# Optimization experiments

Measured on AMD Instinct MI355X. Metric: run time of the kernel, lower is better.

Reference implementation:

```python
import jax, jax.numpy as jnp
import numpy as np

B, N, D, H, E = 32, 512, 512, 8, 4
HD = D // H
EPS = 1e-3  # keras LayerNormalization default epsilon
NEG = -1e9  # keras Softmax masking additive constant


def _ln(x, g, b):
    m = jnp.mean(x, axis=-1, keepdims=True)
    v = jnp.mean(jnp.square(x - m), axis=-1, keepdims=True)
    return (x - m) * jax.lax.rsqrt(v + EPS) * g + b


def setup_inputs() -> dict:
    key = jax.random.key(0)
    ks = jax.random.split(key, 16)
    s = 0.02
    return {
        "x": jax.random.normal(ks[0], (B, N, D), jnp.float32),
        "mask": jax.random.randint(ks[1], (B, 1, N, N), 0, 2) > 0,
        "interaction": jax.random.normal(ks[2], (B, N, N, H), jnp.float32),
        "w_qkv": jax.random.normal(ks[3], (D, 3 * D), jnp.float32) * s,
        "b_qkv": jnp.zeros((3 * D,), jnp.float32),
        "w_out": jax.random.normal(ks[4], (D, D), jnp.float32) * s,
        "b_out": jnp.zeros((D,), jnp.float32),
        "w1": jax.random.normal(ks[5], (D, E * D), jnp.float32) * s,
        "b1": jnp.zeros((E * D,), jnp.float32),
        "w2": jax.random.normal(ks[6], (E * D, D), jnp.float32) * s,
        "b2": jnp.zeros((D,), jnp.float32),
        "g_pre": jnp.ones((D,), jnp.float32), "be_pre": jnp.zeros((D,), jnp.float32),
        "g_post": jnp.ones((D,), jnp.float32), "be_post": jnp.zeros((D,), jnp.float32),
        "g_ffn": jnp.ones((D,), jnp.float32), "be_ffn": jnp.zeros((D,), jnp.float32),
        "g_mid": jnp.ones((E * D,), jnp.float32), "be_mid": jnp.zeros((E * D,), jnp.float32),
    }


def reference(x, mask, interaction, w_qkv, b_qkv, w_out, b_out, w1, b1, w2, b2,
              g_pre, be_pre, g_post, be_post, g_ffn, be_ffn, g_mid, be_mid):
    # pre-LN MHSA
    h = _ln(x, g_pre, be_pre)
    qkv = h @ w_qkv + b_qkv                           # [B,N,3D]
    qkv = qkv.reshape(B, N, 3, H, HD)
    q, k, v = (jnp.transpose(qkv[:, :, i], (0, 2, 1, 3)) for i in range(3))  # [B,H,N,HD]
    scores = jnp.einsum('bhnd,bhmd->bhnm', q, k) / np.sqrt(HD).astype(np.float32)
    scores = scores + jnp.transpose(interaction, (0, 3, 1, 2))  # per-head additive bias
    scores = scores + (1.0 - mask.astype(scores.dtype)) * NEG   # keras Softmax mask semantics
    attn = jax.nn.softmax(scores, axis=-1)
    o = jnp.einsum('bhnm,bhmd->bhnd', attn, v)
    o = jnp.transpose(o, (0, 2, 1, 3)).reshape(B, N, D)
    o = o @ w_out + b_out
    attended = _ln(o, g_post, be_post) + x            # post-MHSA LN then residual
    # FFN with mid-LN
    f = _ln(attended, g_ffn, be_ffn)
    f = jax.nn.gelu(f @ w1 + b1, approximate=False)
    f = _ln(f, g_mid, be_mid)
    f = f @ w2 + b2
    return f + attended
```

## Files before the change

kernel.cpp:

```cpp
#include <hip/hip_runtime.h>
#include <hip/hip_bf16.h>
#include <math.h>

constexpr int CB = 32, CN = 512, CD = 512, CH = 8, CHD = 64;
constexpr float LN_EPS = 1e-3f;

typedef _Float16 half8 __attribute__((ext_vector_type(8)));
typedef float f32x4 __attribute__((ext_vector_type(4)));

__device__ __forceinline__ void async16(const void* g, void* l) {
    __builtin_amdgcn_global_load_lds((const __attribute__((address_space(1))) void*)g,
                                     (__attribute__((address_space(3))) void*)l, 16, 0, 0);
}

__global__ __launch_bounds__(256) void transpose_f16(const float* __restrict__ in,
                                                     _Float16* __restrict__ out,
                                                     int K, int N) {
    __shared__ float t[32][33];
    const int tx = threadIdx.x % 32, ty = threadIdx.x / 32;
    const int n0 = blockIdx.x * 32, k0 = blockIdx.y * 32;
#pragma unroll
    for (int i = 0; i < 4; ++i)
        t[ty + i * 8][tx] = in[(size_t)(k0 + ty + i * 8) * N + n0 + tx];
    __syncthreads();
#pragma unroll
    for (int i = 0; i < 4; ++i)
        out[(size_t)(n0 + ty + i * 8) * K + k0 + tx] = (_Float16)t[tx][ty + i * 8];
}

template<int WIDTH, bool IN_F16, bool OUT_F16, bool ADDRES>
__global__ __launch_bounds__(256) void ln2_kernel(const void* __restrict__ in_,
        const float* __restrict__ g, const float* __restrict__ be,
        const float* __restrict__ res, void* __restrict__ out_) {
    constexpr int NPL = WIDTH / 64;
    const int row = blockIdx.x * 4 + (threadIdx.x >> 6);
    const int lane = threadIdx.x & 63;
    const int c0 = lane * NPL;
    float v[NPL];
    if (IN_F16) {
        const _Float16* p = (const _Float16*)in_ + (size_t)row * WIDTH + c0;
#pragma unroll
        for (int i = 0; i < NPL / 8; ++i) {
            half8 u = *(const half8*)(p + i * 8);
#pragma unroll
            for (int j = 0; j < 8; ++j) v[i * 8 + j] = (float)u[j];
        }
    } else {
        const float* p = (const float*)in_ + (size_t)row * WIDTH + c0;
#pragma unroll
        for (int i = 0; i < NPL / 4; ++i) {
            float4 u = *(const float4*)(p + i * 4);
            v[i * 4 + 0] = u.x; v[i * 4 + 1] = u.y; v[i * 4 + 2] = u.z; v[i * 4 + 3] = u.w;
        }
    }
    float s1 = 0.f, s2 = 0.f;
#pragma unroll
    for (int i = 0; i < NPL; ++i) { s1 += v[i]; s2 += v[i] * v[i]; }
#pragma unroll
    for (int off = 1; off < 64; off <<= 1) { s1 += __shfl_xor(s1, off); s2 += __shfl_xor(s2, off); }
    const float mean = s1 * (1.0f / WIDTH);
    const float var = s2 * (1.0f / WIDTH) - mean * mean;
    const float rstd = rsqrtf(var + LN_EPS);

    float ov[NPL];
#pragma unroll
    for (int i = 0; i < NPL / 4; ++i) {
        float4 gv = *(const float4*)(g + c0 + i * 4);
        float4 bv = *(const float4*)(be + c0 + i * 4);
        ov[i * 4 + 0] = (v[i * 4 + 0] - mean) * rstd * gv.x + bv.x;
        ov[i * 4 + 1] = (v[i * 4 + 1] - mean) * rstd * gv.y + bv.y;
        ov[i * 4 + 2] = (v[i * 4 + 2] - mean) * rstd * gv.z + bv.z;
        ov[i * 4 + 3] = (v[i * 4 + 3] - mean) * rstd * gv.w + bv.w;
    }
    if (ADDRES) {
        const float* rp = res + (size_t)row * WIDTH + c0;
#pragma unroll
        for (int i = 0; i < NPL / 4; ++i) {
            float4 rv = *(const float4*)(rp + i * 4);
            ov[i * 4 + 0] += rv.x; ov[i * 4 + 1] += rv.y; ov[i * 4 + 2] += rv.z; ov[i * 4 + 3] += rv.w;
        }
    }
    if (OUT_F16) {
        _Float16* po = (_Float16*)out_ + (size_t)row * WIDTH + c0;
#pragma unroll
        for (int i = 0; i < NPL / 8; ++i) {
            half8 hv;
#pragma unroll
            for (int j = 0; j < 8; ++j) hv[j] = (_Float16)ov[i * 8 + j];
            *(half8*)(po + i * 8) = hv;
        }
    } else {
        float* po = (float*)out_ + (size_t)row * WIDTH + c0;
#pragma unroll
        for (int i = 0; i < NPL / 4; ++i) {
            float4 w = make_float4(ov[i * 4 + 0], ov[i * 4 + 1], ov[i * 4 + 2], ov[i * 4 + 3]);
            *(float4*)(po + i * 4) = w;
        }
    }
}

__global__ __launch_bounds__(256) void ln_post_ffn(const _Float16* __restrict__ o2,
        const float* __restrict__ x,
        const float* __restrict__ g_post, const float* __restrict__ be_post,
        const float* __restrict__ g_ffn, const float* __restrict__ be_ffn,
        float* __restrict__ attended, _Float16* __restrict__ f) {
    constexpr int NPL = 8;
    const int row = blockIdx.x * 4 + (threadIdx.x >> 6);
    const int lane = threadIdx.x & 63;
    const int c0 = lane * NPL;
    float v[NPL], xv[NPL];
    {
        half8 u = *(const half8*)(o2 + (size_t)row * CD + c0);
#pragma unroll
        for (int j = 0; j < 8; ++j) v[j] = (float)u[j];
        float4 a = *(const float4*)(x + (size_t)row * CD + c0);
        float4 b = *(const float4*)(x + (size_t)row * CD + c0 + 4);
        xv[0] = a.x; xv[1] = a.y; xv[2] = a.z; xv[3] = a.w;
        xv[4] = b.x; xv[5] = b.y; xv[6] = b.z; xv[7] = b.w;
    }
    float s1 = 0.f, s2 = 0.f;
#pragma unroll
    for (int i = 0; i < NPL; ++i) { s1 += v[i]; s2 += v[i] * v[i]; }
#pragma unroll
    for (int off = 1; off < 64; off <<= 1) { s1 += __shfl_xor(s1, off); s2 += __shfl_xor(s2, off); }
    float mean = s1 * (1.0f / CD);
    float rstd = rsqrtf(s2 * (1.0f / CD) - mean * mean + LN_EPS);
    float av[NPL];
#pragma unroll
    for (int i = 0; i < NPL; ++i)
        av[i] = (v[i] - mean) * rstd * g_post[c0 + i] + be_post[c0 + i] + xv[i];
    {
        float4 w0 = make_float4(av[0], av[1], av[2], av[3]);
        float4 w1 = make_float4(av[4], av[5], av[6], av[7]);
        *(float4*)(attended + (size_t)row * CD + c0) = w0;
        *(float4*)(attended + (size_t)row * CD + c0 + 4) = w1;
    }
    s1 = 0.f; s2 = 0.f;
#pragma unroll
    for (int i = 0; i < NPL; ++i) { s1 += av[i]; s2 += av[i] * av[i]; }
#pragma unroll
    for (int off = 1; off < 64; off <<= 1) { s1 += __shfl_xor(s1, off); s2 += __shfl_xor(s2, off); }
    mean = s1 * (1.0f / CD);
    rstd = rsqrtf(s2 * (1.0f / CD) - mean * mean + LN_EPS);
    half8 hv;
#pragma unroll
    for (int i = 0; i < NPL; ++i)
        hv[i] = (_Float16)((av[i] - mean) * rstd * g_ffn[c0 + i] + be_ffn[c0 + i]);
    *(half8*)(f + (size_t)row * CD + c0) = hv;
}

template<bool GELU, bool RES, bool OUT_F16>
__global__ __launch_bounds__(256) void gemm_f16(const _Float16* __restrict__ A,
        const _Float16* __restrict__ Wt, const float* __restrict__ bias,
        const float* __restrict__ res, void* __restrict__ Cout,
        int M, int N, int K) {
    __shared__ __align__(16) char As[2][16384];
    __shared__ __align__(16) char Bs[2][16384];
    const int tid = threadIdx.x;
    const int nbx = N >> 7;
    const int nwg = (M >> 7) * nbx;
    int gb = blockIdx.x;
    gb = (gb & 7) * (nwg >> 3) + (gb >> 3);
    const int by = gb / nbx, bx = gb % nbx;

    const int lane = tid & 63;
    const int wv = tid >> 6;
    const int rsub = lane >> 3;
    const int slot = lane & 7;
    const int chunk = slot ^ rsub;
    const _Float16* Abase = A + (size_t)(by * 128) * K + chunk * 8;
    const _Float16* Bbase = Wt + (size_t)(bx * 128) * K + chunk * 8;

    const int wm = wv >> 1, wn = wv & 1;
    const int lrow = lane & 15;
    const int lk = lane >> 4;
    const int xorv = lane & 7;
    const int aRowB = (wm * 64 + lrow) * 128;
    const int bRowB = (wn * 64 + lrow) * 128;

    f32x4 acc[4][4] = {};

    auto stage = [&](int buf, int k0) {
#pragma unroll
        for (int t = 0; t < 4; ++t) {
            const int rowb = t * 32 + wv * 8;
            async16(Abase + (size_t)(rowb + rsub) * K + k0, As[buf] + rowb * 128);
            async16(Bbase + (size_t)(rowb + rsub) * K + k0, Bs[buf] + rowb * 128);
        }
    };

    const int nsteps = K >> 6;
    stage(0, 0);
    for (int step = 0; step < nsteps; ++step) {
        const int cur = step & 1;
        if (step + 1 < nsteps) {
            stage(cur ^ 1, (step + 1) * 64);
            asm volatile("s_waitcnt vmcnt(8)" ::: "memory");
        } else {
            asm volatile("s_waitcnt vmcnt(0)" ::: "memory");
        }
        __builtin_amdgcn_s_barrier();
#pragma unroll
        for (int kk = 0; kk < 2; ++kk) {
            const int sa = ((kk * 4 + lk) ^ xorv) << 4;
            half8 af[4], bf[4];
#pragma unroll
            for (int mi = 0; mi < 4; ++mi) af[mi] = *(const half8*)(As[cur] + aRowB + mi * 2048 + sa);
#pragma unroll
            for (int ni = 0; ni < 4; ++ni) bf[ni] = *(const half8*)(Bs[cur] + bRowB + ni * 2048 + sa);
#pragma unroll
            for (int mi = 0; mi < 4; ++mi)
#pragma unroll
                for (int ni = 0; ni < 4; ++ni)
                    acc[mi][ni] = __builtin_amdgcn_mfma_f32_16x16x32_f16(af[mi], bf[ni], acc[mi][ni], 0, 0, 0);
        }
        asm volatile("s_waitcnt lgkmcnt(0)" ::: "memory");
        __builtin_amdgcn_s_barrier();
    }

    const int lr4 = (lane >> 4) * 4;
    const int lc = lane & 15;
#pragma unroll
    for (int ni = 0; ni < 4; ++ni) {
        const int colg = bx * 128 + wn * 64 + ni * 16 + lc;
        const float bv = bias[colg];
#pragma unroll
        for (int mi = 0; mi < 4; ++mi) {
            const int rowg = by * 128 + wm * 64 + mi * 16 + lr4;
#pragma unroll
            for (int r = 0; r < 4; ++r) {
                float v = acc[mi][ni][r] + bv;
                if (GELU) v = 0.5f * v * (1.0f + erff(v * 0.70710678118654752440f));
                if (RES) v += res[(size_t)(rowg + r) * N + colg];
                if (OUT_F16) ((_Float16*)Cout)[(size_t)(rowg + r) * N + colg] = (_Float16)v;
                else ((float*)Cout)[(size_t)(rowg + r) * N + colg] = v;
            }
        }
    }
}

__global__ __launch_bounds__(256) void attn_mfma(
        const _Float16* __restrict__ qkv, const float* __restrict__ inter,
        const int* __restrict__ mask, _Float16* __restrict__ o) {
    const int bid = blockIdx.x;
    const int xcd = bid & 7;
    const int s = bid >> 3;
    const int h = s & 7;
    const int qt = (s >> 3) & 7;
    const int b = (s >> 6) * 8 + xcd;
    const int tid = threadIdx.x;
    const int lane = tid & 63;
    const int w = tid >> 6;
    const int l15 = lane & 15, l4 = lane >> 4;

    __shared__ __align__(16) char Qs[8192];
    __shared__ __align__(16) char Ks[8192];
    __shared__ __align__(16) char Vt[8192];
    __shared__ __align__(16) char Ps[8192];

    constexpr size_t QKVROW = 1536;
    {
        const _Float16* Qg = qkv + (size_t)(b * CN + qt * 64) * QKVROW + h * 64;
#pragma unroll
        for (int p = 0; p < 2; ++p) {
            const int f = tid + 256 * p;
            const int r = f >> 3, c = f & 7;
            half8 v = *(const half8*)(Qg + (size_t)r * QKVROW + c * 8);
            *(half8*)(Qs + r * 128 + ((c ^ (r & 7)) << 4)) = v;
        }
    }

    f32x4 acc_o[4] = {};
    float m_run[4] = {-3e38f, -3e38f, -3e38f, -3e38f};
    float l_run[4] = {0.f, 0.f, 0.f, 0.f};

    const int qg0 = qt * 64 + w * 16 + l4 * 4;
    const float* interB[4];
    const int* maskB[4];
#pragma unroll
    for (int r = 0; r < 4; ++r) {
        interB[r] = inter + ((size_t)(b * CN + qg0 + r) * CN) * CH + h;
        maskB[r]  = mask + (size_t)(b * CN + qg0 + r) * CN;
    }

    for (int mt = 0; mt < 8; ++mt) {
        __syncthreads();
        const _Float16* Kg = qkv + (size_t)(b * CN + mt * 64) * QKVROW + 512 + h * 64;
        const _Float16* Vg = Kg + 512;
#pragma unroll
        for (int p = 0; p < 2; ++p) {
            const int f = tid + 256 * p;
            const int r = f >> 3, c = f & 7;
            half8 kv = *(const half8*)(Kg + (size_t)r * QKVROW + c * 8);
            *(half8*)(Ks + r * 128 + ((c ^ (r & 7)) << 4)) = kv;
        }
#pragma unroll
        for (int p = 0; p < 2; ++p) {
            const int f = tid + 256 * p;
            const int m = f >> 3, dc = f & 7;
            half8 vv = *(const half8*)(Vg + (size_t)m * QKVROW + dc * 8);
            const int mc = m >> 3, mo = m & 7;
#pragma unroll
            for (int j = 0; j < 8; ++j) {
                const int d = dc * 8 + j;
                *(_Float16*)(Vt + d * 128 + ((mc ^ (d & 7) ^ dc) << 4) + mo * 2) = vv[j];
            }
        }
        float iv[4][4];
#pragma unroll
        for (int r = 0; r < 4; ++r)
#pragma unroll
            for (int mi = 0; mi < 4; ++mi) {
                const int m = mt * 64 + mi * 16 + l15;
                const float bvv = interB[r][(size_t)m * CH];
                iv[r][mi] = bvv + (maskB[r][m] ? 0.f : -1e9f);
            }
        __syncthreads();

        f32x4 acc_s[4] = {};
#pragma unroll
        for (int step = 0; step < 2; ++step) {
            const int qrow = w * 16 + l15;
            const int ch = step * 4 + l4;
            half8 aq = *(const half8*)(Qs + qrow * 128 + ((ch ^ (qrow & 7)) << 4));
#pragma unroll
            for (int mi = 0; mi < 4; ++mi) {
                const int mrow = mi * 16 + l15;
                half8 bk = *(const half8*)(Ks + mrow * 128 + ((ch ^ (mrow & 7)) << 4));
                acc_s[mi] = __builtin_amdgcn_mfma_f32_16x16x32_f16(aq, bk, acc_s[mi], 0, 0, 0);
            }
        }
#pragma unroll
        for (int r = 0; r < 4; ++r) {
            float pv[4];
            float rmax = -3e38f;
#pragma unroll
            for (int mi = 0; mi < 4; ++mi) {
                float sv = acc_s[mi][r] * 0.125f + iv[r][mi];
                pv[mi] = sv;
                rmax = fmaxf(rmax, sv);
            }
#pragma unroll
            for (int off = 1; off < 16; off <<= 1) rmax = fmaxf(rmax, __shfl_xor(rmax, off));
            const float nm = fmaxf(m_run[r], rmax);
            const float fac = __expf(m_run[r] - nm);
            m_run[r] = nm;
            float ps = 0.f;
#pragma unroll
            for (int mi = 0; mi < 4; ++mi) { float e = __expf(pv[mi] - nm); pv[mi] = e; ps += e; }
#pragma unroll
            for (int off = 1; off < 16; off <<= 1) ps += __shfl_xor(ps, off);
            l_run[r] = l_run[r] * fac + ps;
#pragma unroll
            for (int di = 0; di < 4; ++di) acc_o[di][r] *= fac;
            const int qrow = w * 16 + l4 * 4 + r;
#pragma unroll
            for (int mi = 0; mi < 4; ++mi) {
                const int m = mi * 16 + l15;
                *(_Float16*)(Ps + qrow * 128 + (((m >> 3) ^ (qrow & 7)) << 4) + (m & 7) * 2) = (_Float16)pv[mi];
            }
        }
#pragma unroll
        for (int step = 0; step < 2; ++step) {
            const int qrow = w * 16 + l15;
            const int ch = step * 4 + l4;
            half8 ap = *(const half8*)(Ps + qrow * 128 + ((ch ^ (qrow & 7)) << 4));
#pragma unroll
            for (int di = 0; di < 4; ++di) {
                const int drow = di * 16 + l15;
                half8 bv = *(const half8*)(Vt + drow * 128 + ((ch ^ (drow & 7) ^ (drow >> 3)) << 4));
                acc_o[di] = __builtin_amdgcn_mfma_f32_16x16x32_f16(ap, bv, acc_o[di], 0, 0, 0);
            }
        }
    }
    _Float16* orow = o + (size_t)(b * CN + qt * 64 + w * 16 + l4 * 4) * CD + h * 64 + l15;
#pragma unroll
    for (int r = 0; r < 4; ++r) {
        const float inv = 1.0f / l_run[r];
#pragma unroll
        for (int di = 0; di < 4; ++di)
            orow[(size_t)r * CD + di * 16] = (_Float16)(acc_o[di][r] * inv);
    }
}

extern "C" void kernel_launch(void* const* d_in, const int* in_sizes, int n_in,
                              void* d_out, int out_size, void* d_ws, size_t ws_size,
                              hipStream_t stream) {
    const float* x      = (const float*)d_in[0];
    const int*   mask   = (const int*)d_in[1];
    const float* inter  = (const float*)d_in[2];
    const float* w_qkv  = (const float*)d_in[3];
    const float* b_qkv  = (const float*)d_in[4];
    const float* w_out  = (const float*)d_in[5];
    const float* b_out  = (const float*)d_in[6];
    const float* w1     = (const float*)d_in[7];
    const float* b1     = (const float*)d_in[8];
    const float* w2     = (const float*)d_in[9];
    const float* b2     = (const float*)d_in[10];
    const float* g_pre  = (const float*)d_in[11];
    const float* be_pre = (const float*)d_in[12];
    const float* g_post = (const float*)d_in[13];
    const float* be_post= (const float*)d_in[14];
    const float* g_ffn  = (const float*)d_in[15];
    const float* be_ffn = (const float*)d_in[16];
    const float* g_mid  = (const float*)d_in[17];
    const float* be_mid = (const float*)d_in[18];
    float* out = (float*)d_out;

    char* ws = (char*)d_ws;
    const size_t MB = 1ull << 20;
    _Float16* wt_qkv = (_Float16*)(ws + 0 * MB);
    _Float16* wt_out = (_Float16*)(ws + 2 * MB);
    _Float16* wt_w1  = (_Float16*)(ws + 3 * MB);
    _Float16* wt_w2  = (_Float16*)(ws + 5 * MB);
    float*    attended = (float*)(ws + 8 * MB);
    _Float16* o2h    = (_Float16*)(ws + 40 * MB);
    _Float16* f1b    = (_Float16*)(ws + 64 * MB);
    _Float16* qkvb   = (_Float16*)(ws + 128 * MB);
    _Float16* hb     = (_Float16*)(ws + 176 * MB);
    _Float16* ob     = (_Float16*)(ws + 192 * MB);
    _Float16* fb     = (_Float16*)(ws + 208 * MB);

    const int M = CB * CN;

    transpose_f16<<<dim3(1536 / 32, 512 / 32), 256, 0, stream>>>(w_qkv, wt_qkv, 512, 1536);
    transpose_f16<<<dim3(512 / 32, 512 / 32), 256, 0, stream>>>(w_out, wt_out, 512, 512);
    transpose_f16<<<dim3(2048 / 32, 512 / 32), 256, 0, stream>>>(w1, wt_w1, 512, 2048);
    transpose_f16<<<dim3(512 / 32, 2048 / 32), 256, 0, stream>>>(w2, wt_w2, 2048, 512);

    ln2_kernel<512, false, true, false><<<M / 4, 256, 0, stream>>>(x, g_pre, be_pre, nullptr, hb);
    gemm_f16<false, false, true><<<(M / 128) * (1536 / 128), 256, 0, stream>>>(
        hb, wt_qkv, b_qkv, nullptr, qkvb, M, 1536, 512);
    attn_mfma<<<CB * 8 * 8, 256, 0, stream>>>(qkvb, inter, mask, ob);
    gemm_f16<false, false, true><<<(M / 128) * (512 / 128), 256, 0, stream>>>(
        ob, wt_out, b_out, nullptr, o2h, M, 512, 512);
    ln_post_ffn<<<M / 4, 256, 0, stream>>>(o2h, x, g_post, be_post, g_ffn, be_ffn, attended, fb);
    gemm_f16<true, false, true><<<(M / 128) * (2048 / 128), 256, 0, stream>>>(
        fb, wt_w1, b1, nullptr, f1b, M, 2048, 512);
    ln2_kernel<2048, true, true, false><<<M / 4, 256, 0, stream>>>(f1b, g_mid, be_mid, nullptr, f1b);
    gemm_f16<false, true, false><<<(M / 128) * (512 / 128), 256, 0, stream>>>(
        f1b, wt_w2, b2, attended, out, M, 512, 2048);
}
```

Before: 439.4 us.

## Fold mid-FFN LayerNorm into GEMM epilogues and process two query tiles per attention block

Result: slower. 601.0 us (+36.8%).

```diff
diff --git a/kernel.cpp b/kernel.cpp
--- a/kernel.cpp
+++ b/kernel.cpp
@@ -13,7 +13,9 @@
                                      (__attribute__((address_space(3))) void*)l, 16, 0, 0);
 }
 
+template<bool SCALE>
 __global__ __launch_bounds__(256) void transpose_f16(const float* __restrict__ in,
+                                                     const float* __restrict__ g,
                                                      _Float16* __restrict__ out,
                                                      int K, int N) {
     __shared__ float t[32][33];
@@ -23,9 +25,24 @@
     for (int i = 0; i < 4; ++i)
         t[ty + i * 8][tx] = in[(size_t)(k0 + ty + i * 8) * N + n0 + tx];
     __syncthreads();
+    const float gs = SCALE ? g[k0 + tx] : 1.0f;
 #pragma unroll
     for (int i = 0; i < 4; ++i)
-        out[(size_t)(n0 + ty + i * 8) * K + k0 + tx] = (_Float16)t[tx][ty + i * 8];
+        out[(size_t)(n0 + ty + i * 8) * K + k0 + tx] = (_Float16)(t[tx][ty + i * 8] * gs);
+}
+
+__global__ __launch_bounds__(256) void colsum_w2(const float* __restrict__ w2,
+        const float* __restrict__ g, const float* __restrict__ be,
+        float* __restrict__ S1, float* __restrict__ S2) {
+    const int n = blockIdx.x * 256 + threadIdx.x;
+    float s1 = 0.f, s2 = 0.f;
+    for (int c = 0; c < 4 * CD; ++c) {
+        const float w = w2[(size_t)c * CD + n];
+        s1 += g[c] * w;
+        s2 += be[c] * w;
+    }
+    S1[n] = s1;
+    S2[n] = s2;
 }
 
 template<int WIDTH, bool IN_F16, bool OUT_F16, bool ADDRES>
@@ -149,11 +166,13 @@
     *(half8*)(f + (size_t)row * CD + c0) = hv;
 }
 
-template<bool GELU, bool RES, bool OUT_F16>
+template<bool GELU, bool RES, bool OUT_F16, bool STATS, bool MIDLN>
 __global__ __launch_bounds__(256) void gemm_f16(const _Float16* __restrict__ A,
         const _Float16* __restrict__ Wt, const float* __restrict__ bias,
         const float* __restrict__ res, void* __restrict__ Cout,
-        int M, int N, int K) {
+        int M, int N, int K,
+        float* __restrict__ rowsum, float* __restrict__ rowsumsq,
+        const float* __restrict__ S1, const float* __restrict__ S2) {
     __shared__ __align__(16) char As[2][16384];
     __shared__ __align__(16) char Bs[2][16384];
     const int tid = threadIdx.x;
@@ -220,21 +239,68 @@
 
     const int lr4 = (lane >> 4) * 4;
     const int lc = lane & 15;
+
+    float muv[4][4], rhov[4][4];
+    if (MIDLN) {
+#pragma unroll
+        for (int mi = 0; mi < 4; ++mi)
+#pragma unroll
+            for (int r = 0; r < 4; ++r) {
+                const int row = by * 128 + wm * 64 + mi * 16 + lr4 + r;
+                const float mu = rowsum[row] * (1.0f / (4 * CD));
+                const float var = rowsumsq[row] * (1.0f / (4 * CD)) - mu * mu;
+                const float rho = rsqrtf(var + LN_EPS);
+                muv[mi][r] = mu * rho;
+                rhov[mi][r] = rho;
+            }
+    }
+
+    float st1[4][4] = {}, st2[4][4] = {};
 #pragma unroll
     for (int ni = 0; ni < 4; ++ni) {
         const int colg = bx * 128 + wn * 64 + ni * 16 + lc;
         const float bv = bias[colg];
+        const float s1v = MIDLN ? S1[colg] : 0.f;
+        const float s2v = MIDLN ? S2[colg] : 0.f;
 #pragma unroll
         for (int mi = 0; mi < 4; ++mi) {
             const int rowg = by * 128 + wm * 64 + mi * 16 + lr4;
 #pragma unroll
             for (int r = 0; r < 4; ++r) {
-                float v = acc[mi][ni][r] + bv;
-                if (GELU) v = 0.5f * v * (1.0f + erff(v * 0.70710678118654752440f));
+                float v;
+                if (MIDLN) {
+                    v = rhov[mi][r] * acc[mi][ni][r] - muv[mi][r] * s1v + s2v + bv;
+                } else {
+                    v = acc[mi][ni][r] + bv;
+                    if (GELU) v = 0.5f * v * (1.0f + erff(v * 0.70710678118654752440f));
+                }
+                if (STATS) { st1[mi][r] += v; st2[mi][r] += v * v; }
                 if (RES) v += res[(size_t)(rowg + r) * N + colg];
                 if (OUT_F16) ((_Float16*)Cout)[(size_t)(rowg + r) * N + colg] = (_Float16)v;
                 else ((float*)Cout)[(size_t)(rowg + r) * N + colg] = v;
             }
+        }
+    }
+    if (STATS) {
+#pragma unroll
+        for (int mi = 0; mi < 4; ++mi)
+#pragma unroll
+            for (int r = 0; r < 4; ++r) {
+#pragma unroll
+                for (int off = 1; off < 16; off <<= 1) {
+                    st1[mi][r] += __shfl_xor(st1[mi][r], off);
+                    st2[mi][r] += __shfl_xor(st2[mi][r], off);
+                }
+            }
+        if (lc == 0) {
+#pragma unroll
+            for (int mi = 0; mi < 4; ++mi)
+#pragma unroll
+                for (int r = 0; r < 4; ++r) {
+                    const int row = by * 128 + wm * 64 + mi * 16 + lr4 + r;
+                    atomicAdd(&rowsum[row], st1[mi][r]);
+                    atomicAdd(&rowsumsq[row], st2[mi][r]);
+                }
         }
     }
 }
@@ -246,35 +312,39 @@
     const int xcd = bid & 7;
     const int s = bid >> 3;
     const int h = s & 7;
-    const int qt = (s >> 3) & 7;
-    const int b = (s >> 6) * 8 + xcd;
+    const int qp = (s >> 3) & 3;
+    const int b = (s >> 5) * 8 + xcd;
     const int tid = threadIdx.x;
     const int lane = tid & 63;
     const int w = tid >> 6;
     const int l15 = lane & 15, l4 = lane >> 4;
 
-    __shared__ __align__(16) char Qs[8192];
+    __shared__ __align__(16) char Qs[2][8192];
     __shared__ __align__(16) char Ks[8192];
     __shared__ __align__(16) char Vt[8192];
     __shared__ __align__(16) char Ps[8192];
 
     constexpr size_t QKVROW = 1536;
-    {
-        const _Float16* Qg = qkv + (size_t)(b * CN + qt * 64) * QKVROW + h * 64;
+#pragma unroll
+    for (int tt = 0; tt < 2; ++tt) {
+        const _Float16* Qg = qkv + (size_t)(b * CN + (qp * 2 + tt) * 64) * QKVROW + h * 64;
 #pragma unroll
         for (int p = 0; p < 2; ++p) {
             const int f = tid + 256 * p;
             const int r = f >> 3, c = f & 7;
             half8 v = *(const half8*)(Qg + (size_t)r * QKVROW + c * 8);
-            *(half8*)(Qs + r * 128 + ((c ^ (r & 7)) << 4)) = v;
-        }
-    }
-
-    f32x4 acc_o[4] = {};
-    float m_run[4] = {-3e38f, -3e38f, -3e38f, -3e38f};
-    float l_run[4] = {0.f, 0.f, 0.f, 0.f};
-
-    const int qg0 = qt * 64 + w * 16 + l4 * 4;
+            *(half8*)(Qs[tt] + r * 128 + ((c ^ (r & 7)) << 4)) = v;
+        }
+    }
+
+    f32x4 acc_o[2][4] = {};
+    float m_run[2][4], l_run[2][4];
+#pragma unroll
+    for (int tt = 0; tt < 2; ++tt)
+#pragma unroll
+        for (int r = 0; r < 4; ++r) { m_run[tt][r] = -3e38f; l_run[tt][r] = 0.f; }
+
+    const int qg0 = qp * 128 + w * 16 + l4 * 4;
     const float* interB[4];
     const int* maskB[4];
 #pragma unroll
@@ -282,6 +352,8 @@
         interB[r] = inter + ((size_t)(b * CN + qg0 + r) * CN) * CH + h;
         maskB[r]  = mask + (size_t)(b * CN + qg0 + r) * CN;
     }
+    constexpr size_t IOFF = (size_t)64 * CN * CH;
+    constexpr size_t MOFF = (size_t)64 * CN;
 
     for (int mt = 0; mt < 8; ++mt) {
         __syncthreads();
@@ -306,80 +378,88 @@
                 *(_Float16*)(Vt + d * 128 + ((mc ^ (d & 7) ^ dc) << 4) + mo * 2) = vv[j];
             }
         }
-        float iv[4][4];
-#pragma unroll
-        for (int r = 0; r < 4; ++r)
-#pragma unroll
-            for (int mi = 0; mi < 4; ++mi) {
-                const int m = mt * 64 + mi * 16 + l15;
-                const float bvv = interB[r][(size_t)m * CH];
-                iv[r][mi] = bvv + (maskB[r][m] ? 0.f : -1e9f);
-            }
+        float iv[2][4][4];
+#pragma unroll
+        for (int tt = 0; tt < 2; ++tt)
+#pragma unroll
+            for (int r = 0; r < 4; ++r)
+#pragma unroll
+                for (int mi = 0; mi < 4; ++mi) {
+                    const int m = mt * 64 + mi * 16 + l15;
+                    const float bvv = interB[r][(size_t)m * CH + tt * IOFF];
+                    iv[tt][r][mi] = bvv + (maskB[r][m + tt * MOFF] ? 0.f : -1e9f);
+                }
         __syncthreads();
 
-        f32x4 acc_s[4] = {};
-#pragma unroll
-        for (int step = 0; step < 2; ++step) {
-            const int qrow = w * 16 + l15;
-            const int ch = step * 4 + l4;
-            half8 aq = *(const half8*)(Qs + qrow * 128 + ((ch ^ (qrow & 7)) << 4));
-#pragma unroll
-            for (int mi = 0; mi < 4; ++mi) {
-                const int mrow = mi * 16 + l15;
-                half8 bk = *(const half8*)(Ks + mrow * 128 + ((ch ^ (mrow & 7)) << 4));
-                acc_s[mi] = __builtin_amdgcn_mfma_f32_16x16x32_f16(aq, bk, acc_s[mi], 0, 0, 0);
-            }
-        }
+#pragma unroll
+        for (int tt = 0; tt < 2; ++tt) {
+            f32x4 acc_s[4] = {};
+#pragma unroll
+            for (int step = 0; step < 2; ++step) {
+                const int qrow = w * 16 + l15;
+                const int ch = step * 4 + l4;
+                half8 aq = *(const half8*)(Qs[tt] + qrow * 128 + ((ch ^ (qrow & 7)) << 4));
+#pragma unroll
+                for (int mi = 0; mi < 4; ++mi) {
+                    const int mrow = mi * 16 + l15;
+                    half8 bk = *(const half8*)(Ks + mrow * 128 + ((ch ^ (mrow & 7)) << 4));
+                    acc_s[mi] = __builtin_amdgcn_mfma_f32_16x16x32_f16(aq, bk, acc_s[mi], 0, 0, 0);
+                }
+            }
+#pragma unroll
+            for (int r = 0; r < 4; ++r) {
+                float pv[4];
+                float rmax = -3e38f;
+#pragma unroll
+                for (int mi = 0; mi < 4; ++mi) {
+                    float sv = acc_s[mi][r] * 0.125f + iv[tt][r][mi];
+                    pv[mi] = sv;
+                    rmax = fmaxf(rmax, sv);
+                }
+#pragma unroll
+                for (int off = 1; off < 16; off <<= 1) rmax = fmaxf(rmax, __shfl_xor(rmax, off));
+                const float nm = fmaxf(m_run[tt][r], rmax);
+                const float fac = __expf(m_run[tt][r] - nm);
+                m_run[tt][r] = nm;
+                float ps = 0.f;
+#pragma unroll
+                for (int mi = 0; mi < 4; ++mi) { float e = __expf(pv[mi] - nm); pv[mi] = e; ps += e; }
+#pragma unroll
+                for (int off = 1; off < 16; off <<= 1) ps += __shfl_xor(ps, off);
+                l_run[tt][r] = l_run[tt][r] * fac + ps;
+#pragma unroll
+                for (int di = 0; di < 4; ++di) acc_o[tt][di][r] *= fac;
+                const int qrow = w * 16 + l4 * 4 + r;
+#pragma unroll
+                for (int mi = 0; mi < 4; ++mi) {
+                    const int m = mi * 16 + l15;
+                    *(_Float16*)(Ps + qrow * 128 + (((m >> 3) ^ (qrow & 7)) << 4) + (m & 7) * 2) = (_Float16)pv[mi];
+                }
+            }
+#pragma unroll
+            for (int step = 0; step < 2; ++step) {
+                const int qrow = w * 16 + l15;
+                const int ch = step * 4 + l4;
+                half8 ap = *(const half8*)(Ps + qrow * 128 + ((ch ^ (qrow & 7)) << 4));
+#pragma unroll
+                for (int di = 0; di < 4; ++di) {
+                    const int drow = di * 16 + l15;
+                    half8 bv = *(const half8*)(Vt + drow * 128 + ((ch ^ (drow & 7) ^ (drow >> 3)) << 4));
+                    acc_o[tt][di] = __builtin_amdgcn_mfma_f32_16x16x32_f16(ap, bv, acc_o[tt][di], 0, 0, 0);
+                }
+            }
+        }
+    }
+#pragma unroll
+    for (int tt = 0; tt < 2; ++tt) {
+        _Float16* orow = o + (size_t)(b * CN + (qp * 2 + tt) * 64 + w * 16 + l4 * 4) * CD + h * 64 + l15;
 #pragma unroll
         for (int r = 0; r < 4; ++r) {
-            float pv[4];
-            float rmax = -3e38f;
-#pragma unroll
-            for (int mi = 0; mi < 4; ++mi) {
-                float sv = acc_s[mi][r] * 0.125f + iv[r][mi];
-                pv[mi] = sv;
-                rmax = fmaxf(rmax, sv);
-            }
-#pragma unroll
-            for (int off = 1; off < 16; off <<= 1) rmax = fmaxf(rmax, __shfl_xor(rmax, off));
-            const float nm = fmaxf(m_run[r], rmax);
-            const float fac = __expf(m_run[r] - nm);
-            m_run[r] = nm;
-            float ps = 0.f;
-#pragma unroll
-            for (int mi = 0; mi < 4; ++mi) { float e = __expf(pv[mi] - nm); pv[mi] = e; ps += e; }
-#pragma unroll
-            for (int off = 1; off < 16; off <<= 1) ps += __shfl_xor(ps, off);
-            l_run[r] = l_run[r] * fac + ps;
-#pragma unroll
-            for (int di = 0; di < 4; ++di) acc_o[di][r] *= fac;
-            const int qrow = w * 16 + l4 * 4 + r;
-#pragma unroll
-            for (int mi = 0; mi < 4; ++mi) {
-                const int m = mi * 16 + l15;
-                *(_Float16*)(Ps + qrow * 128 + (((m >> 3) ^ (qrow & 7)) << 4) + (m & 7) * 2) = (_Float16)pv[mi];
-            }
-        }
-#pragma unroll
-        for (int step = 0; step < 2; ++step) {
-            const int qrow = w * 16 + l15;
-            const int ch = step * 4 + l4;
-            half8 ap = *(const half8*)(Ps + qrow * 128 + ((ch ^ (qrow & 7)) << 4));
-#pragma unroll
-            for (int di = 0; di < 4; ++di) {
-                const int drow = di * 16 + l15;
-                half8 bv = *(const half8*)(Vt + drow * 128 + ((ch ^ (drow & 7) ^ (drow >> 3)) << 4));
-                acc_o[di] = __builtin_amdgcn_mfma_f32_16x16x32_f16(ap, bv, acc_o[di], 0, 0, 0);
-            }
-        }
-    }
-    _Float16* orow = o + (size_t)(b * CN + qt * 64 + w * 16 + l4 * 4) * CD + h * 64 + l15;
-#pragma unroll
-    for (int r = 0; r < 4; ++r) {
-        const float inv = 1.0f / l_run[r];
-#pragma unroll
-        for (int di = 0; di < 4; ++di)
-            orow[(size_t)r * CD + di * 16] = (_Float16)(acc_o[di][r] * inv);
+            const float inv = 1.0f / l_run[tt][r];
+#pragma unroll
+            for (int di = 0; di < 4; ++di)
+                orow[(size_t)r * CD + di * 16] = (_Float16)(acc_o[tt][di][r] * inv);
+        }
     }
 }
 
@@ -415,6 +495,10 @@
     _Float16* wt_w2  = (_Float16*)(ws + 5 * MB);
     float*    attended = (float*)(ws + 8 * MB);
     _Float16* o2h    = (_Float16*)(ws + 40 * MB);
+    float*    rowsum   = (float*)(ws + 56 * MB);
+    float*    rowsumsq = (float*)(ws + 56 * MB + (64 << 10));
+    float*    S1buf    = (float*)(ws + 57 * MB);
+    float*    S2buf    = (float*)(ws + 57 * MB + (4 << 10));
     _Float16* f1b    = (_Float16*)(ws + 64 * MB);
     _Float16* qkvb   = (_Float16*)(ws + 128 * MB);
     _Float16* hb     = (_Float16*)(ws + 176 * MB);
@@ -423,21 +507,22 @@
 
     const int M = CB * CN;
 
-    transpose_f16<<<dim3(1536 / 32, 512 / 32), 256, 0, stream>>>(w_qkv, wt_qkv, 512, 1536);
-    transpose_f16<<<dim3(512 / 32, 512 / 32), 256, 0, stream>>>(w_out, wt_out, 512, 512);
-    transpose_f16<<<dim3(2048 / 32, 512 / 32), 256, 0, stream>>>(w1, wt_w1, 512, 2048);
-    transpose_f16<<<dim3(512 / 32, 2048 / 32), 256, 0, stream>>>(w2, wt_w2, 2048, 512);
+    transpose_f16<false><<<dim3(1536 / 32, 512 / 32), 256, 0, stream>>>(w_qkv, nullptr, wt_qkv, 512, 1536);
+    transpose_f16<false><<<dim3(512 / 32, 512 / 32), 256, 0, stream>>>(w_out, nullptr, wt_out, 512, 512);
+    transpose_f16<false><<<dim3(2048 / 32, 512 / 32), 256, 0, stream>>>(w1, nullptr, wt_w1, 512, 2048);
+    transpose_f16<true><<<dim3(512 / 32, 2048 / 32), 256, 0, stream>>>(w2, g_mid, wt_w2, 2048, 512);
+    colsum_w2<<<2, 256, 0, stream>>>(w2, g_mid, be_mid, S1buf, S2buf);
+    hipMemsetAsync(rowsum, 0, 128 << 10, stream);
 
     ln2_kernel<512, false, true, false><<<M / 4, 256, 0, stream>>>(x, g_pre, be_pre, nullptr, hb);
-    gemm_f16<false, false, true><<<(M / 128) * (1536 / 128), 256, 0, stream>>>(
-        hb, wt_qkv, b_qkv, nullptr, qkvb, M, 1536, 512);
-    attn_mfma<<<CB * 8 * 8, 256, 0, stream>>>(qkvb, inter, mask, ob);
-    gemm_f16<false, false, true><<<(M / 128) * (512 / 128), 256, 0, stream>>>(
-        ob, wt_out, b_out, nullptr, o2h, M, 512, 512);
+    gemm_f16<false, false, true, false, false><<<(M / 128) * (1536 / 128), 256, 0, stream>>>(
+        hb, wt_qkv, b_qkv, nullptr, qkvb, M, 1536, 512, nullptr, nullptr, nullptr, nullptr);
+    attn_mfma<<<CB * 8 * 4, 256, 0, stream>>>(qkvb, inter, mask, ob);
+    gemm_f16<false, false, true, false, false><<<(M / 128) * (512 / 128), 256, 0, stream>>>(
+        ob, wt_out, b_out, nullptr, o2h, M, 512, 512, nullptr, nullptr, nullptr, nullptr);
     ln_post_ffn<<<M / 4, 256, 0, stream>>>(o2h, x, g_post, be_post, g_ffn, be_ffn, attended, fb);
-    gemm_f16<true, false, true><<<(M / 128) * (2048 / 128), 256, 0, stream>>>(
-        fb, wt_w1, b1, nullptr, f1b, M, 2048, 512);
-    ln2_kernel<2048, true, true, false><<<M / 4, 256, 0, stream>>>(f1b, g_mid, be_mid, nullptr, f1b);
-    gemm_f16<false, true, false><<<(M / 128) * (512 / 128), 256, 0, stream>>>(
-        f1b, wt_w2, b2, attended, out, M, 512, 2048);
-}
+    gemm_f16<true, false, true, true, false><<<(M / 128) * (2048 / 128), 256, 0, stream>>>(
+        fb, wt_w1, b1, nullptr, f1b, M, 2048, 512, rowsum, rowsumsq, nullptr, nullptr);
+    gemm_f16<false, true, false, false, true><<<(M / 128) * (512 / 128), 256, 0, stream>>>(
+        f1b, wt_w2, b2, attended, out, M, 512, 2048, rowsum, rowsumsq, S1buf, S2buf);
+}
```
